# Optimization experiments

Hardware: AMD Instinct MI355X
Metric: run time of the kernel (lower is better)

Reference implementation:

```python
import jax, jax.numpy as jnp
import numpy as np

B, C, H, W = 16, 512, 96, 96
CQK = C // 8


def setup_inputs() -> dict:
    key = jax.random.key(0)
    ks = jax.random.split(key, 8)
    s = 0.05  # keep projections / logits in a numerically sane range
    return {
        "x": jax.random.normal(ks[0], (B, C, H, W), jnp.float32),
        "Wq": jax.random.normal(ks[1], (CQK, C), jnp.float32) * s,
        "bq": jax.random.normal(ks[2], (CQK,), jnp.float32) * s,
        "Wk": jax.random.normal(ks[3], (CQK, C), jnp.float32) * s,
        "bk": jax.random.normal(ks[4], (CQK,), jnp.float32) * s,
        "Wv": jax.random.normal(ks[5], (C, C), jnp.float32) * s,
        "bv": jax.random.normal(ks[6], (C,), jnp.float32) * s,
        "gamma": jax.random.normal(ks[7], (1,), jnp.float32),
    }


def reference(x, Wq, bq, Wk, bk, Wv, bv, gamma):
    # 1x1 convs are per-pixel GEMMs
    q = jnp.einsum("bchw,oc->bohw", x, Wq) + bq[None, :, None, None]
    k = jnp.einsum("bchw,oc->bohw", x, Wk) + bk[None, :, None, None]
    v = jnp.einsum("bchw,oc->bohw", x, Wv) + bv[None, :, None, None]

    h = x.shape[2]
    # column affinities: query at (h,w) vs keys at (u,w)  -> [B,H,H,W]
    eH = jnp.einsum("bchw,bcuw->buhw", q, k)
    # exclude the center pixel from the column set (ca_forward uses H-1 column entries)
    center = jnp.arange(h)[:, None] == jnp.arange(h)[None, :]  # [u,h]
    eH = jnp.where(center[None, :, :, None], -jnp.inf, eH)
    # row affinities: query at (h,w) vs keys at (h,v) -> [B,W,H,W]
    eW = jnp.einsum("bchw,bchv->bvhw", q, k)

    energy = jnp.concatenate([eH, eW], axis=1)      # [B, H+W, H, W]
    att = jax.nn.softmax(energy, axis=1)
    aH, aW = att[:, :h], att[:, h:]

    # criss-cross aggregation (ca_map)
    out = jnp.einsum("buhw,bcuw->bchw", aH, v) + jnp.einsum("bvhw,bchv->bchw", aW, v)
    return gamma[0] * out + x
```

## Files before the change

### kernel.cpp

```cpp
#include <hip/hip_runtime.h>
#include <hip/hip_bf16.h>
#include <stdint.h>

#define BB 16
#define CC 512
#define CQK 64
#define HH 96
#define WW 96
#define HW (HH*WW)
#define NPIX (BB*HW)

typedef float f32x4 __attribute__((ext_vector_type(4)));
typedef short s16x8 __attribute__((ext_vector_type(8)));

__device__ __forceinline__ unsigned short f2bf(float f){
    unsigned u = __float_as_uint(f);
    unsigned r = (u + 0x7FFFu + ((u >> 16) & 1u)) >> 16;
    return (unsigned short)r;
}
__device__ __forceinline__ float bf2f(unsigned short h){
    return __uint_as_float(((unsigned)h) << 16);
}
__device__ __forceinline__ void gload16(const void* g, void* l){
    __builtin_amdgcn_global_load_lds((const __attribute__((address_space(1))) unsigned int*)g,
                                     (__attribute__((address_space(3))) unsigned int*)l, 16, 0, 0);
}

__global__ __launch_bounds__(256) void k_convw(const float* Wq, const float* Wk, const float* Wv,
                                               unsigned short* Wqkv){
    int o = blockIdx.x, t = threadIdx.x;
    const float* src = (o < 64) ? (Wq + (size_t)o*512)
                     : (o < 128) ? (Wk + (size_t)(o-64)*512)
                                 : (Wv + (size_t)(o-128)*512);
    unsigned short* dst = Wqkv + (size_t)o*512;
    for (int c = t; c < 512; c += 256) dst[c] = f2bf(src[c]);
}

__global__ __launch_bounds__(256) void k_xT(const float* __restrict__ x,
                                            unsigned short* __restrict__ xT,
                                            unsigned short* __restrict__ xbf){
    __shared__ float tile[64][65];
    int b = blockIdx.z, ct = blockIdx.y, nt = blockIdx.x;
    int t = threadIdx.x;
    const float* xb = x + ((size_t)(b*CC + ct*64))*HW + (size_t)nt*64;
    unsigned short* d2 = xbf + ((size_t)(b*CC + ct*64))*HW + (size_t)nt*64;
    #pragma unroll
    for (int s = 0; s < 4; s++){
        int idx = s*256 + t;
        int ci = idx >> 4, n4 = (idx & 15)*4;
        f32x4 vv = *(const f32x4*)(xb + (size_t)ci*HW + n4);
        *(f32x4*)(&tile[ci][n4]) = vv;
        ushort4 u; u.x=f2bf(vv[0]); u.y=f2bf(vv[1]); u.z=f2bf(vv[2]); u.w=f2bf(vv[3]);
        *(ushort4*)(d2 + (size_t)ci*HW + n4) = u;
    }
    __syncthreads();
    unsigned short* dst = xT + ((size_t)b*HW + (size_t)nt*64)*512 + ct*64;
    #pragma unroll
    for (int s = 0; s < 4; s++){
        int idx = s*256 + t;
        int ni = idx >> 4, c0 = (idx & 15)*4;
        ushort4 u;
        u.x = f2bf(tile[c0  ][ni]); u.y = f2bf(tile[c0+1][ni]);
        u.z = f2bf(tile[c0+2][ni]); u.w = f2bf(tile[c0+3][ni]);
        *(ushort4*)(dst + (size_t)ni*512 + c0) = u;
    }
}

__device__ __forceinline__ void stage_tiles(const unsigned short* Ag, const unsigned short* Bg,
                                            unsigned short* As, unsigned short* Bs,
                                            int wv, int kt){
    #pragma unroll
    for (int s = 0; s < 4; s++){
        int chunk = wv*4 + s;
        gload16(Ag + (size_t)chunk*8*512 + (size_t)kt*64, As + chunk*512);
        gload16(Bg + (size_t)chunk*8*512 + (size_t)kt*64, Bs + chunk*512);
    }
}

__global__ __launch_bounds__(256) void k_gemm(const unsigned short* __restrict__ Wqkv,
                                              const unsigned short* __restrict__ xT,
                                              const float* __restrict__ bq, const float* __restrict__ bk,
                                              const float* __restrict__ bv,
                                              unsigned short* __restrict__ q_t,
                                              unsigned short* __restrict__ k_t,
                                              unsigned short* __restrict__ v){
    __shared__ unsigned short As[2][128*64];
    __shared__ unsigned short Bs[2][128*64];
    int b = blockIdx.z, mt = blockIdx.y, nt = blockIdx.x;
    int t = threadIdx.x, wv = t >> 6, lane = t & 63;
    int wr = wv >> 1, wc = wv & 1;
    const unsigned short* Ag = Wqkv + (size_t)(mt*128)*512
                               + (size_t)(lane>>3)*512 + (size_t)(((lane&7) ^ (lane>>3))*8);
    const unsigned short* Bg = xT + ((size_t)b*HW + (size_t)nt*128)*512
                               + (size_t)(lane>>3)*512 + (size_t)(((lane&7) ^ (lane>>3))*8);
    f32x4 acc[4][4] = {};
    stage_tiles(Ag, Bg, As[0], Bs[0], wv, 0);
    stage_tiles(Ag, Bg, As[1], Bs[1], wv, 1);
    #pragma unroll
    for (int kt = 0; kt < 8; kt++){
        int cur = kt & 1;
        if (kt < 7) asm volatile("s_waitcnt vmcnt(8)" ::: "memory");
        else        asm volatile("s_waitcnt vmcnt(0)" ::: "memory");
        __builtin_amdgcn_s_barrier();
        asm volatile("" ::: "memory");
        __builtin_amdgcn_s_setprio(1);
        #pragma unroll
        for (int kk = 0; kk < 2; kk++){
            int xr = (((kk*4 + (lane>>4)) ^ (lane&7)) << 3);
            s16x8 af[4], bfr[4];
            #pragma unroll
            for (int i = 0; i < 4; i++) af[i]  = *(const s16x8*)(&As[cur][(wr*64 + i*16 + (lane&15))*64 + xr]);
            #pragma unroll
            for (int j = 0; j < 4; j++) bfr[j] = *(const s16x8*)(&Bs[cur][(wc*64 + j*16 + (lane&15))*64 + xr]);
            #pragma unroll
            for (int i = 0; i < 4; i++)
                #pragma unroll
                for (int j = 0; j < 4; j++)
                    acc[i][j] = __builtin_amdgcn_mfma_f32_16x16x32_bf16(af[i], bfr[j], acc[i][j], 0, 0, 0);
        }
        __builtin_amdgcn_s_setprio(0);
        asm volatile("" ::: "memory");
        __builtin_amdgcn_s_barrier();
        asm volatile("" ::: "memory");
        if (kt < 6) stage_tiles(Ag, Bg, As[cur], Bs[cur], wv, kt+2);
    }
    if (mt == 0){
        const float* bias = (wr == 0) ? bq : bk;
        unsigned short* dst = (wr == 0) ? q_t : k_t;
        #pragma unroll
        for (int i = 0; i < 4; i++){
            int m0 = i*16 + (lane >> 4)*4;
            f32x4 bb = *(const f32x4*)(bias + m0);
            #pragma unroll
            for (int j = 0; j < 4; j++){
                int n = nt*128 + wc*64 + j*16 + (lane & 15);
                ushort4 u;
                u.x = f2bf(acc[i][j][0] + bb[0]);
                u.y = f2bf(acc[i][j][1] + bb[1]);
                u.z = f2bf(acc[i][j][2] + bb[2]);
                u.w = f2bf(acc[i][j][3] + bb[3]);
                *(ushort4*)(dst + ((size_t)b*HW + n)*64 + m0) = u;
            }
        }
    } else {
        #pragma unroll
        for (int i = 0; i < 4; i++){
            int c0 = (mt-1)*128 + wr*64 + i*16 + (lane >> 4)*4;
            f32x4 bb = *(const f32x4*)(bv + c0);
            #pragma unroll
            for (int j = 0; j < 4; j++){
                int n = nt*128 + wc*64 + j*16 + (lane & 15);
                #pragma unroll
                for (int r = 0; r < 4; r++)
                    v[((size_t)b*CC + c0 + r)*HW + n] = f2bf(acc[i][j][r] + bb[r]);
            }
        }
    }
}

__global__ __launch_bounds__(256) void k_vT(const unsigned short* v, unsigned short* vT){
    __shared__ unsigned int tile[96][97];
    int b = blockIdx.y, c = blockIdx.x, t = threadIdx.x;
    const unsigned short* src = v + ((size_t)b*CC + c)*HW;
    unsigned short* dst = vT + ((size_t)b*CC + c)*HW;
    for (int idx = t; idx < HW; idx += 256){
        tile[idx/96][idx%96] = src[idx];
    }
    __syncthreads();
    for (int idx = t; idx < HW; idx += 256){
        int w = idx/96, h = idx%96;
        dst[idx] = (unsigned short)tile[h][w];
    }
}

__global__ __launch_bounds__(128) void k_energy(const unsigned short* __restrict__ q_t,
                                                const unsigned short* __restrict__ k_t,
                                                float* __restrict__ E){
    __shared__ unsigned short qs[96*72], ks[96*72];
    int b = blockIdx.y, y = blockIdx.x;
    int t = threadIdx.x, wv = t >> 6, lane = t & 63;
    int modeW = (y >= 96);
    size_t base; size_t rstride;
    if (!modeW){ base = ((size_t)b*HW + y)*64;            rstride = (size_t)96*64; }
    else       { base = ((size_t)b*HW + (size_t)(y-96)*96)*64; rstride = 64; }
    #pragma unroll
    for (int s = 0; s < 6; s++){
        int chunk = s*128 + t;
        int row = chunk >> 3, c8 = chunk & 7;
        *(s16x8*)(&qs[row*72 + c8*8]) = *(const s16x8*)(q_t + base + (size_t)row*rstride + c8*8);
        *(s16x8*)(&ks[row*72 + c8*8]) = *(const s16x8*)(k_t + base + (size_t)row*rstride + c8*8);
    }
    __syncthreads();
    f32x4 acc[6][3] = {};
    #pragma unroll
    for (int kk = 0; kk < 2; kk++){
        int ko = kk*32 + (lane >> 4)*8;
        s16x8 af[6], bfr[3];
        #pragma unroll
        for (int i = 0; i < 6; i++) af[i]  = *(const s16x8*)(&qs[(i*16 + (lane&15))*72 + ko]);
        #pragma unroll
        for (int j = 0; j < 3; j++) bfr[j] = *(const s16x8*)(&ks[(wv*48 + j*16 + (lane&15))*72 + ko]);
        #pragma unroll
        for (int i = 0; i < 6; i++)
            #pragma unroll
            for (int j = 0; j < 3; j++)
                acc[i][j] = __builtin_amdgcn_mfma_f32_16x16x32_bf16(af[i], bfr[j], acc[i][j], 0, 0, 0);
    }
    #pragma unroll
    for (int i = 0; i < 6; i++){
        #pragma unroll
        for (int j = 0; j < 3; j++){
            #pragma unroll
            for (int r = 0; r < 4; r++){
                int row = i*16 + (lane >> 4)*4 + r;
                int col = wv*48 + j*16 + (lane & 15);
                float val = acc[i][j][r];
                size_t pix; int jcol;
                if (!modeW){ pix = (size_t)b*HW + (size_t)row*96 + y; jcol = col;
                             if (row == col) val = -1e30f; }
                else       { pix = (size_t)b*HW + (size_t)(y-96)*96 + row; jcol = 96 + col; }
                E[pix*192 + jcol] = val;
            }
        }
    }
}

__global__ __launch_bounds__(256) void k_softmax(const float* __restrict__ E,
                                                 unsigned short* __restrict__ att){
    int t = threadIdx.x;
    int g = t & 7;
    size_t pix = (size_t)blockIdx.x*32 + (t >> 3);
    const float* e = E + pix*192;
    f32x4 vals[6];
    float m = -3e38f;
    #pragma unroll
    for (int s = 0; s < 6; s++){
        vals[s] = *(const f32x4*)(e + s*32 + g*4);
        #pragma unroll
        for (int q = 0; q < 4; q++) m = fmaxf(m, vals[s][q]);
    }
    #pragma unroll
    for (int d = 1; d < 8; d <<= 1) m = fmaxf(m, __shfl_xor(m, d, 64));
    float sum = 0.f;
    #pragma unroll
    for (int s = 0; s < 6; s++){
        #pragma unroll
        for (int q = 0; q < 4; q++){ vals[s][q] = __expf(vals[s][q] - m); sum += vals[s][q]; }
    }
    #pragma unroll
    for (int d = 1; d < 8; d <<= 1) sum += __shfl_xor(sum, d, 64);
    float inv = 1.0f / sum;
    unsigned short* o = att + pix*192;
    #pragma unroll
    for (int s = 0; s < 6; s++){
        ushort4 u;
        u.x = f2bf(vals[s][0]*inv); u.y = f2bf(vals[s][1]*inv);
        u.z = f2bf(vals[s][2]*inv); u.w = f2bf(vals[s][3]*inv);
        *(ushort4*)(o + s*32 + g*4) = u;
    }
}

template<int MODEW>
__global__ __launch_bounds__(256) void k_agg(const unsigned short* __restrict__ V,
                                             const unsigned short* __restrict__ att,
                                             unsigned short* __restrict__ OUT){
    __shared__ unsigned short As[256*104];
    __shared__ unsigned short Bs[96*104];
    int b = blockIdx.y, xx = blockIdx.x;
    int mh = xx & 1, y = xx >> 1;
    int t = threadIdx.x, wvv = t >> 6, lane = t & 63;
    const unsigned short* Ag = V + ((size_t)b*CC + (size_t)mh*256)*HW + (size_t)y*96;
    const unsigned short* Bg; size_t bstride;
    if (!MODEW){ Bg = att + ((size_t)b*HW + y)*192;                 bstride = (size_t)96*192; }
    else       { Bg = att + ((size_t)b*HW + (size_t)y*96)*192 + 96; bstride = 192; }
    #pragma unroll
    for (int s = 0; s < 12; s++){
        int chunk = s*256 + t;
        int row = chunk/12, c8 = chunk%12;
        *(s16x8*)(&As[row*104 + c8*8]) = *(const s16x8*)(Ag + (size_t)row*HW + c8*8);
    }
    #pragma unroll
    for (int s = 0; s < 5; s++){
        int chunk = s*256 + t;
        if (chunk < 1152){
            int row = chunk/12, c8 = chunk%12;
            *(s16x8*)(&Bs[row*104 + c8*8]) = *(const s16x8*)(Bg + (size_t)row*bstride + c8*8);
        }
    }
    __syncthreads();
    f32x4 acc[4][6] = {};
    #pragma unroll
    for (int kk = 0; kk < 3; kk++){
        int ko = kk*32 + (lane >> 4)*8;
        s16x8 af[4], bfr[6];
        #pragma unroll
        for (int i = 0; i < 4; i++) af[i]  = *(const s16x8*)(&As[(wvv*64 + i*16 + (lane&15))*104 + ko]);
        #pragma unroll
        for (int j = 0; j < 6; j++) bfr[j] = *(const s16x8*)(&Bs[(j*16 + (lane&15))*104 + ko]);
        #pragma unroll
        for (int i = 0; i < 4; i++)
            #pragma unroll
            for (int j = 0; j < 6; j++)
                acc[i][j] = __builtin_amdgcn_mfma_f32_16x16x32_bf16(af[i], bfr[j], acc[i][j], 0, 0, 0);
    }
    #pragma unroll
    for (int i = 0; i < 4; i++){
        #pragma unroll
        for (int j = 0; j < 6; j++){
            int col = j*16 + (lane & 15);
            #pragma unroll
            for (int r = 0; r < 4; r++){
                int c = mh*256 + wvv*64 + i*16 + (lane >> 4)*4 + r;
                OUT[((size_t)b*CC + c)*HW + (size_t)y*96 + col] = f2bf(acc[i][j][r]);
            }
        }
    }
}

__global__ __launch_bounds__(256) void k_combine(const unsigned short* __restrict__ outH,
                                                 const unsigned short* __restrict__ outW,
                                                 const unsigned short* __restrict__ xbf,
                                                 const float* __restrict__ gamma,
                                                 float* __restrict__ out){
    __shared__ float tile[96][97];
    int b = blockIdx.y, c = blockIdx.x, t = threadIdx.x;
    const unsigned short* hp = outH + ((size_t)b*CC + c)*HW;
    #pragma unroll
    for (int s = 0; s < 9; s++){
        int idx = s*1024 + t*4;
        ushort4 u = *(const ushort4*)(hp + idx);
        int r = idx/96, cc = idx%96;
        tile[r][cc] = bf2f(u.x); tile[r][cc+1] = bf2f(u.y);
        tile[r][cc+2] = bf2f(u.z); tile[r][cc+3] = bf2f(u.w);
    }
    __syncthreads();
    float g = gamma[0];
    size_t base = ((size_t)b*CC + c)*HW;
    #pragma unroll
    for (int s = 0; s < 9; s++){
        int idx = s*1024 + t*4;
        ushort4 uw = *(const ushort4*)(outW + base + idx);
        ushort4 ux = *(const ushort4*)(xbf + base + idx);
        int h = idx/96, w = idx%96;
        f32x4 o;
        o[0] = g*(bf2f(uw.x) + tile[w  ][h]) + bf2f(ux.x);
        o[1] = g*(bf2f(uw.y) + tile[w+1][h]) + bf2f(ux.y);
        o[2] = g*(bf2f(uw.z) + tile[w+2][h]) + bf2f(ux.z);
        o[3] = g*(bf2f(uw.w) + tile[w+3][h]) + bf2f(ux.w);
        *(f32x4*)(out + base + idx) = o;
    }
}

extern "C" void kernel_launch(void* const* d_in, const int* in_sizes, int n_in,
                              void* d_out, int out_size, void* d_ws, size_t ws_size,
                              hipStream_t stream){
    const float* x     = (const float*)d_in[0];
    const float* Wq    = (const float*)d_in[1];
    const float* bq    = (const float*)d_in[2];
    const float* Wk    = (const float*)d_in[3];
    const float* bk    = (const float*)d_in[4];
    const float* Wv    = (const float*)d_in[5];
    const float* bv    = (const float*)d_in[6];
    const float* gamma = (const float*)d_in[7];

    constexpr size_t SZ_BIG = (size_t)BB*CC*HW*2;
    constexpr size_t SZ_QK  = (size_t)BB*HW*64*2;
    constexpr size_t SZ_ATT = (size_t)BB*HW*192*2;

    char* ws = (char*)d_ws;
    unsigned short* xT   = (unsigned short*)(ws);
    unsigned short* v    = (unsigned short*)(ws + SZ_BIG);
    unsigned short* xbf  = (unsigned short*)(ws + 2*SZ_BIG);
    unsigned short* q_t  = (unsigned short*)(ws + 3*SZ_BIG);
    unsigned short* k_t  = (unsigned short*)(ws + 3*SZ_BIG + SZ_QK);
    unsigned short* att  = (unsigned short*)(ws + 3*SZ_BIG + 2*SZ_QK);
    unsigned short* Wqkv = (unsigned short*)(ws + 3*SZ_BIG + 2*SZ_QK + SZ_ATT);

    float*          E    = (float*)d_out;
    unsigned short* vT   = (unsigned short*)((char*)d_out + SZ_BIG);
    float*          out  = (float*)d_out;
    unsigned short* outH = xT;
    unsigned short* outW = v;

    k_convw   <<<dim3(640),        dim3(256), 0, stream>>>(Wq, Wk, Wv, Wqkv);
    k_xT      <<<dim3(144, 8, 16), dim3(256), 0, stream>>>(x, xT, xbf);
    k_gemm    <<<dim3(72, 5, 16),  dim3(256), 0, stream>>>(Wqkv, xT, bq, bk, bv, q_t, k_t, v);
    k_vT      <<<dim3(512, 16),    dim3(256), 0, stream>>>(v, vT);
    k_energy  <<<dim3(192, 16),    dim3(128), 0, stream>>>(q_t, k_t, E);
    k_softmax <<<dim3(4608),       dim3(256), 0, stream>>>(E, att);
    k_agg<0>  <<<dim3(192, 16),    dim3(256), 0, stream>>>(vT, att, outH);
    k_agg<1>  <<<dim3(192, 16),    dim3(256), 0, stream>>>(v,  att, outW);
    k_combine <<<dim3(512, 16),    dim3(256), 0, stream>>>(outH, outW, xbf, gamma, out);
}
```

Before: 737.0 us.

## Merge small kernels into combined launches and store energies as bf16

Merges the weight-conversion and x-transpose kernels into one launch, fuses the V transpose with the energy kernel through block-index dispatch, and merges the two aggregation launches into one grid. The energy kernel now uses 256 threads in a 2x2 wave tiling, and the energy matrix is stored in bf16 instead of fp32, halving energy write and read traffic. The softmax is rewritten to read contiguous 24-element bf16 chunks per thread. Launch overhead and tail effects are reduced, but bf16 logits lose some precision before the softmax.

Measured after the change: 695.7 us. 1.06x faster.

```diff
diff --git a/kernel.cpp b/kernel.cpp
--- a/kernel.cpp
+++ b/kernel.cpp
@@ -26,22 +26,23 @@
                                      (__attribute__((address_space(3))) unsigned int*)l, 16, 0, 0);
 }
 
-__global__ __launch_bounds__(256) void k_convw(const float* Wq, const float* Wk, const float* Wv,
-                                               unsigned short* Wqkv){
-    int o = blockIdx.x, t = threadIdx.x;
-    const float* src = (o < 64) ? (Wq + (size_t)o*512)
-                     : (o < 128) ? (Wk + (size_t)(o-64)*512)
-                                 : (Wv + (size_t)(o-128)*512);
-    unsigned short* dst = Wqkv + (size_t)o*512;
-    for (int c = t; c < 512; c += 256) dst[c] = f2bf(src[c]);
-}
-
-__global__ __launch_bounds__(256) void k_xT(const float* __restrict__ x,
-                                            unsigned short* __restrict__ xT,
-                                            unsigned short* __restrict__ xbf){
+__global__ __launch_bounds__(256) void k_prep(const float* __restrict__ Wq, const float* __restrict__ Wk,
+                                              const float* __restrict__ Wv, unsigned short* __restrict__ Wqkv,
+                                              const float* __restrict__ x,
+                                              unsigned short* __restrict__ xT,
+                                              unsigned short* __restrict__ xbf){
     __shared__ float tile[64][65];
-    int b = blockIdx.z, ct = blockIdx.y, nt = blockIdx.x;
-    int t = threadIdx.x;
+    int bid = blockIdx.x, t = threadIdx.x;
+    if (bid < 640){
+        const float* src = (bid < 64) ? (Wq + (size_t)bid*512)
+                         : (bid < 128) ? (Wk + (size_t)(bid-64)*512)
+                                       : (Wv + (size_t)(bid-128)*512);
+        unsigned short* dst = Wqkv + (size_t)bid*512;
+        for (int c = t; c < 512; c += 256) dst[c] = f2bf(src[c]);
+        return;
+    }
+    int r = bid - 640;
+    int nt = r % 144, ct = (r/144) & 7, b = r / 1152;
     const float* xb = x + ((size_t)(b*CC + ct*64))*HW + (size_t)nt*64;
     unsigned short* d2 = xbf + ((size_t)(b*CC + ct*64))*HW + (size_t)nt*64;
     #pragma unroll
@@ -158,120 +159,131 @@
     }
 }
 
-__global__ __launch_bounds__(256) void k_vT(const unsigned short* v, unsigned short* vT){
-    __shared__ unsigned int tile[96][97];
-    int b = blockIdx.y, c = blockIdx.x, t = threadIdx.x;
-    const unsigned short* src = v + ((size_t)b*CC + c)*HW;
-    unsigned short* dst = vT + ((size_t)b*CC + c)*HW;
-    for (int idx = t; idx < HW; idx += 256){
-        tile[idx/96][idx%96] = src[idx];
-    }
-    __syncthreads();
-    for (int idx = t; idx < HW; idx += 256){
-        int w = idx/96, h = idx%96;
-        dst[idx] = (unsigned short)tile[h][w];
-    }
-}
-
-__global__ __launch_bounds__(128) void k_energy(const unsigned short* __restrict__ q_t,
-                                                const unsigned short* __restrict__ k_t,
-                                                float* __restrict__ E){
-    __shared__ unsigned short qs[96*72], ks[96*72];
-    int b = blockIdx.y, y = blockIdx.x;
-    int t = threadIdx.x, wv = t >> 6, lane = t & 63;
+__global__ __launch_bounds__(256) void k_vt_energy(const unsigned short* __restrict__ v,
+                                                   unsigned short* __restrict__ vT,
+                                                   const unsigned short* __restrict__ q_t,
+                                                   const unsigned short* __restrict__ k_t,
+                                                   unsigned short* __restrict__ E){
+    __shared__ char smem[96*97*4];
+    int bid = blockIdx.x, t = threadIdx.x;
+    if (bid < 8192){
+        unsigned int (*tile)[97] = (unsigned int(*)[97])smem;
+        int b = bid >> 9, c = bid & 511;
+        const unsigned short* src = v + ((size_t)b*CC + c)*HW;
+        unsigned short* dst = vT + ((size_t)b*CC + c)*HW;
+        for (int idx = t; idx < HW; idx += 256){
+            tile[idx/96][idx%96] = src[idx];
+        }
+        __syncthreads();
+        for (int idx = t; idx < HW; idx += 256){
+            int w = idx/96, h = idx%96;
+            dst[idx] = (unsigned short)tile[h][w];
+        }
+        return;
+    }
+    int idx2 = bid - 8192;
+    int y = idx2 % 192, b = idx2 / 192;
+    unsigned short* qs = (unsigned short*)smem;
+    unsigned short* ks = qs + 96*72;
+    int wv = t >> 6, lane = t & 63;
+    int wrow = wv >> 1, wcol = wv & 1;
     int modeW = (y >= 96);
-    size_t base; size_t rstride;
-    if (!modeW){ base = ((size_t)b*HW + y)*64;            rstride = (size_t)96*64; }
+    size_t base, rstride;
+    if (!modeW){ base = ((size_t)b*HW + y)*64;                 rstride = (size_t)96*64; }
     else       { base = ((size_t)b*HW + (size_t)(y-96)*96)*64; rstride = 64; }
     #pragma unroll
-    for (int s = 0; s < 6; s++){
-        int chunk = s*128 + t;
+    for (int s = 0; s < 3; s++){
+        int chunk = s*256 + t;
         int row = chunk >> 3, c8 = chunk & 7;
         *(s16x8*)(&qs[row*72 + c8*8]) = *(const s16x8*)(q_t + base + (size_t)row*rstride + c8*8);
         *(s16x8*)(&ks[row*72 + c8*8]) = *(const s16x8*)(k_t + base + (size_t)row*rstride + c8*8);
     }
     __syncthreads();
-    f32x4 acc[6][3] = {};
+    f32x4 acc[3][3] = {};
     #pragma unroll
     for (int kk = 0; kk < 2; kk++){
         int ko = kk*32 + (lane >> 4)*8;
-        s16x8 af[6], bfr[3];
-        #pragma unroll
-        for (int i = 0; i < 6; i++) af[i]  = *(const s16x8*)(&qs[(i*16 + (lane&15))*72 + ko]);
-        #pragma unroll
-        for (int j = 0; j < 3; j++) bfr[j] = *(const s16x8*)(&ks[(wv*48 + j*16 + (lane&15))*72 + ko]);
-        #pragma unroll
-        for (int i = 0; i < 6; i++)
+        s16x8 af[3], bfr[3];
+        #pragma unroll
+        for (int i = 0; i < 3; i++) af[i]  = *(const s16x8*)(&qs[(wrow*48 + i*16 + (lane&15))*72 + ko]);
+        #pragma unroll
+        for (int j = 0; j < 3; j++) bfr[j] = *(const s16x8*)(&ks[(wcol*48 + j*16 + (lane&15))*72 + ko]);
+        #pragma unroll
+        for (int i = 0; i < 3; i++)
             #pragma unroll
             for (int j = 0; j < 3; j++)
                 acc[i][j] = __builtin_amdgcn_mfma_f32_16x16x32_bf16(af[i], bfr[j], acc[i][j], 0, 0, 0);
     }
     #pragma unroll
-    for (int i = 0; i < 6; i++){
+    for (int i = 0; i < 3; i++){
         #pragma unroll
         for (int j = 0; j < 3; j++){
             #pragma unroll
             for (int r = 0; r < 4; r++){
-                int row = i*16 + (lane >> 4)*4 + r;
-                int col = wv*48 + j*16 + (lane & 15);
+                int row = wrow*48 + i*16 + (lane >> 4)*4 + r;
+                int col = wcol*48 + j*16 + (lane & 15);
                 float val = acc[i][j][r];
                 size_t pix; int jcol;
                 if (!modeW){ pix = (size_t)b*HW + (size_t)row*96 + y; jcol = col;
                              if (row == col) val = -1e30f; }
                 else       { pix = (size_t)b*HW + (size_t)(y-96)*96 + row; jcol = 96 + col; }
-                E[pix*192 + jcol] = val;
+                E[pix*192 + jcol] = f2bf(val);
             }
         }
     }
 }
 
-__global__ __launch_bounds__(256) void k_softmax(const float* __restrict__ E,
+__global__ __launch_bounds__(256) void k_softmax(const unsigned short* __restrict__ E,
                                                  unsigned short* __restrict__ att){
     int t = threadIdx.x;
     int g = t & 7;
     size_t pix = (size_t)blockIdx.x*32 + (t >> 3);
-    const float* e = E + pix*192;
-    f32x4 vals[6];
+    const unsigned short* e = E + pix*192 + g*24;
+    s16x8 a[3];
+    a[0] = *(const s16x8*)(e);
+    a[1] = *(const s16x8*)(e + 8);
+    a[2] = *(const s16x8*)(e + 16);
+    float vals[24];
     float m = -3e38f;
     #pragma unroll
-    for (int s = 0; s < 6; s++){
-        vals[s] = *(const f32x4*)(e + s*32 + g*4);
-        #pragma unroll
-        for (int q = 0; q < 4; q++) m = fmaxf(m, vals[s][q]);
-    }
+    for (int s = 0; s < 3; s++)
+        #pragma unroll
+        for (int q = 0; q < 8; q++){
+            float f = bf2f((unsigned short)a[s][q]);
+            vals[s*8+q] = f;
+            m = fmaxf(m, f);
+        }
     #pragma unroll
     for (int d = 1; d < 8; d <<= 1) m = fmaxf(m, __shfl_xor(m, d, 64));
     float sum = 0.f;
     #pragma unroll
-    for (int s = 0; s < 6; s++){
-        #pragma unroll
-        for (int q = 0; q < 4; q++){ vals[s][q] = __expf(vals[s][q] - m); sum += vals[s][q]; }
-    }
+    for (int q = 0; q < 24; q++){ vals[q] = __expf(vals[q] - m); sum += vals[q]; }
     #pragma unroll
     for (int d = 1; d < 8; d <<= 1) sum += __shfl_xor(sum, d, 64);
     float inv = 1.0f / sum;
-    unsigned short* o = att + pix*192;
-    #pragma unroll
-    for (int s = 0; s < 6; s++){
-        ushort4 u;
-        u.x = f2bf(vals[s][0]*inv); u.y = f2bf(vals[s][1]*inv);
-        u.z = f2bf(vals[s][2]*inv); u.w = f2bf(vals[s][3]*inv);
-        *(ushort4*)(o + s*32 + g*4) = u;
-    }
-}
-
-template<int MODEW>
-__global__ __launch_bounds__(256) void k_agg(const unsigned short* __restrict__ V,
+    unsigned short* o = att + pix*192 + g*24;
+    #pragma unroll
+    for (int s = 0; s < 3; s++){
+        s16x8 u;
+        #pragma unroll
+        for (int q = 0; q < 8; q++) u[q] = (short)f2bf(vals[s*8+q]*inv);
+        *(s16x8*)(o + s*8) = u;
+    }
+}
+
+__global__ __launch_bounds__(256) void k_agg(const unsigned short* __restrict__ v,
+                                             const unsigned short* __restrict__ vT,
                                              const unsigned short* __restrict__ att,
-                                             unsigned short* __restrict__ OUT){
+                                             unsigned short* __restrict__ outH,
+                                             unsigned short* __restrict__ outW){
     __shared__ unsigned short As[256*104];
     __shared__ unsigned short Bs[96*104];
     int b = blockIdx.y, xx = blockIdx.x;
-    int mh = xx & 1, y = xx >> 1;
+    int modeW = xx & 1, mh = (xx >> 1) & 1, y = xx >> 2;
     int t = threadIdx.x, wvv = t >> 6, lane = t & 63;
-    const unsigned short* Ag = V + ((size_t)b*CC + (size_t)mh*256)*HW + (size_t)y*96;
+    const unsigned short* Ag = (modeW ? v : vT) + ((size_t)b*CC + (size_t)mh*256)*HW + (size_t)y*96;
     const unsigned short* Bg; size_t bstride;
-    if (!MODEW){ Bg = att + ((size_t)b*HW + y)*192;                 bstride = (size_t)96*192; }
+    if (!modeW){ Bg = att + ((size_t)b*HW + y)*192;                 bstride = (size_t)96*192; }
     else       { Bg = att + ((size_t)b*HW + (size_t)y*96)*192 + 96; bstride = 192; }
     #pragma unroll
     for (int s = 0; s < 12; s++){
@@ -303,6 +315,7 @@
             for (int j = 0; j < 6; j++)
                 acc[i][j] = __builtin_amdgcn_mfma_f32_16x16x32_bf16(af[i], bfr[j], acc[i][j], 0, 0, 0);
     }
+    unsigned short* OUT = modeW ? outW : outH;
     #pragma unroll
     for (int i = 0; i < 4; i++){
         #pragma unroll
@@ -376,19 +389,16 @@
     unsigned short* att  = (unsigned short*)(ws + 3*SZ_BIG + 2*SZ_QK);
     unsigned short* Wqkv = (unsigned short*)(ws + 3*SZ_BIG + 2*SZ_QK + SZ_ATT);
 
-    float*          E    = (float*)d_out;
+    unsigned short* E    = (unsigned short*)d_out;
     unsigned short* vT   = (unsigned short*)((char*)d_out + SZ_BIG);
     float*          out  = (float*)d_out;
     unsigned short* outH = xT;
     unsigned short* outW = v;
 
-    k_convw   <<<dim3(640),        dim3(256), 0, stream>>>(Wq, Wk, Wv, Wqkv);
-    k_xT      <<<dim3(144, 8, 16), dim3(256), 0, stream>>>(x, xT, xbf);
-    k_gemm    <<<dim3(72, 5, 16),  dim3(256), 0, stream>>>(Wqkv, xT, bq, bk, bv, q_t, k_t, v);
-    k_vT      <<<dim3(512, 16),    dim3(256), 0, stream>>>(v, vT);
-    k_energy  <<<dim3(192, 16),    dim3(128), 0, stream>>>(q_t, k_t, E);
-    k_softmax <<<dim3(4608),       dim3(256), 0, stream>>>(E, att);
-    k_agg<0>  <<<dim3(192, 16),    dim3(256), 0, stream>>>(vT, att, outH);
-    k_agg<1>  <<<dim3(192, 16),    dim3(256), 0, stream>>>(v,  att, outW);
-    k_combine <<<dim3(512, 16),    dim3(256), 0, stream>>>(outH, outW, xbf, gamma, out);
-}
+    k_prep      <<<dim3(19072),   dim3(256), 0, stream>>>(Wq, Wk, Wv, Wqkv, x, xT, xbf);
+    k_gemm      <<<dim3(72, 5, 16),dim3(256), 0, stream>>>(Wqkv, xT, bq, bk, bv, q_t, k_t, v);
+    k_vt_energy <<<dim3(11264),   dim3(256), 0, stream>>>(v, vT, q_t, k_t, E);
+    k_softmax   <<<dim3(4608),    dim3(256), 0, stream>>>(E, att);
+    k_agg       <<<dim3(384, 16), dim3(256), 0, stream>>>(v, vT, att, outH, outW);
+    k_combine   <<<dim3(512, 16), dim3(256), 0, stream>>>(outH, outW, xbf, gamma, out);
+}
```
